# Kernel optimization log

Measured on AMD Instinct MI355X. Metric: run time of the kernel, lower is better.

Reference implementation:

```python
import jax, jax.numpy as jnp
import numpy as np

HEAD_SIZE = 64
EMB_SIZE = 1024
B, T = 8, 2048


def setup_inputs() -> dict:
    key = jax.random.key(0)
    k_x, k_q, k_k, k_v, k_m = jax.random.split(key, 5)
    X = jax.random.normal(k_x, (B, T, EMB_SIZE), dtype=jnp.float32)
    # nn.Linear(emb, head, bias=False) weights have shape (head, emb)
    s = EMB_SIZE ** -0.5
    Wq = jax.random.uniform(k_q, (HEAD_SIZE, EMB_SIZE), jnp.float32, -s, s)
    Wk = jax.random.uniform(k_k, (HEAD_SIZE, EMB_SIZE), jnp.float32, -s, s)
    Wv = jax.random.uniform(k_v, (HEAD_SIZE, EMB_SIZE), jnp.float32, -s, s)
    padding_mask = jax.random.randint(k_m, (B, T), 0, 2).astype(bool)
    # ensure no row is fully masked (would yield NaN softmax)
    padding_mask = padding_mask.at[:, 0].set(False)
    return {"X": X, "Wq": Wq, "Wk": Wk, "Wv": Wv, "padding_mask": padding_mask}


def reference(X, Wq, Wk, Wv, padding_mask):
    # X: (B,T,C); W*: (H,C); padding_mask: (B,T) bool, True = masked key
    C = X.shape[-1]
    Q = jnp.einsum('btc,hc->bth', X, Wq)
    K = jnp.einsum('btc,hc->bth', X, Wk)
    V = jnp.einsum('btc,hc->bth', X, Wv)
    # NOTE: source scales by emb_size**-0.5 (C), not head_size**-0.5
    wei = jnp.einsum('bth,bsh->bts', Q, K) * (C ** -0.5)  # (B,T,T)
    wei = jnp.where(padding_mask[:, None, :], -jnp.inf, wei)
    wei = jax.nn.softmax(wei, axis=-1)  # dropout disabled (eval mode)
    out = jnp.einsum('bts,bsh->bth', wei, V)  # (B,T,H)
    return out
```

## Files before the change

### kernel.cpp

```cpp
#include <hip/hip_runtime.h>
#include <hip/hip_bf16.h>
#include <math.h>


#define T_SEQ 2048
#define EMB 1024
#define HS 64
#define NB 8

typedef __attribute__((ext_vector_type(8))) short short8;
typedef __attribute__((ext_vector_type(4))) float f32x4;
typedef __attribute__((ext_vector_type(2))) unsigned int uint2_t;
typedef unsigned short ushort_t;

static __device__ inline ushort_t f2bf(float f) {
  union { float f; unsigned u; } v; v.f = f;
  unsigned r = v.u + 0x7FFF + ((v.u >> 16) & 1);
  return (ushort_t)(r >> 16);
}
static __device__ inline unsigned pk2(float a, float b) {
  return (unsigned)f2bf(a) | ((unsigned)f2bf(b) << 16);
}
static __device__ inline void lds_barrier() {
  asm volatile("s_waitcnt lgkmcnt(0)" ::: "memory");
  __builtin_amdgcn_s_barrier();
}

#define GL16(gp, lp)                                                 \
  __builtin_amdgcn_global_load_lds(                                  \
      (const __attribute__((address_space(1))) void*)(gp),           \
      (__attribute__((address_space(3))) void*)(lp), 16, 0, 0)

__global__ __launch_bounds__(256) void convw_kernel(
    const float* __restrict__ Wq, const float* __restrict__ Wk,
    const float* __restrict__ Wv, ushort_t* __restrict__ Wb) {
  const int m = blockIdx.x >> 4;
  const int blk = blockIdx.x & 15;
  const float* src = (m == 0) ? Wq : (m == 1) ? Wk : Wv;
  const float scale = (m == 0) ? 0.03125f * 1.44269504f : 1.0f;
  const int base = blk * 4096 + threadIdx.x * 16;
  ushort_t* dst = Wb + m * 65536;
  ushort_t tmp[16];
#pragma unroll
  for (int j = 0; j < 4; ++j) {
    float4 x = *(const float4*)(src + base + j * 4);
    tmp[j * 4 + 0] = f2bf(x.x * scale);
    tmp[j * 4 + 1] = f2bf(x.y * scale);
    tmp[j * 4 + 2] = f2bf(x.z * scale);
    tmp[j * 4 + 3] = f2bf(x.w * scale);
  }
  *(short8*)(dst + base) = *(short8*)tmp;
  *(short8*)(dst + base + 8) = *(short8*)(tmp + 8);
}

__global__ __launch_bounds__(256) void proj_kernel(
    const float* __restrict__ X, const ushort_t* __restrict__ Wb,
    ushort_t* __restrict__ Qb, ushort_t* __restrict__ Kb,
    ushort_t* __restrict__ Vtb) {
  __shared__ __align__(16) ushort_t Xs[2][64 * 128];
  const int tid = threadIdx.x;
  const int lane = tid & 63, w = tid >> 6;
  const int l15 = lane & 15, hi = lane >> 4;
  const long rbase = (long)blockIdx.x * 64;

  const ushort_t* Wrow[3];
#pragma unroll
  for (int t = 0; t < 3; ++t) {
    const int ht = 3 * w + t, m = ht >> 2, hs = ht & 3;
    Wrow[t] = Wb + m * 65536 + (hs * 16 + l15) * 1024 + hi * 8;
  }

  short8 wfA[6], wfB[6], wfC[6], wfD[6];
  auto loadw = [&](short8 (&dst)[6], int s) {
#pragma unroll
    for (int t = 0; t < 3; ++t) {
      dst[2 * t + 0] = *(const short8*)(Wrow[t] + s * 64);
      dst[2 * t + 1] = *(const short8*)(Wrow[t] + s * 64 + 32);
    }
  };
  loadw(wfA, 0); loadw(wfB, 1); loadw(wfC, 2);

  float4 xrA[8], xrB[8];
  auto stage_load = [&](float4 (&xr)[8], int c) {
#pragma unroll
    for (int j = 0; j < 8; ++j) {
      const int F = j * 256 + tid;
      const int row = F >> 5, c4 = F & 31;
      xr[j] = *(const float4*)(X + (rbase + row) * EMB + c * 128 + c4 * 4);
    }
  };
  auto stage_write = [&](float4 (&xr)[8], int buf) {
    ushort_t* Xd = Xs[buf];
#pragma unroll
    for (int j = 0; j < 8; ++j) {
      const int F = j * 256 + tid;
      const int row = F >> 5, c4 = F & 31;
      uint2_t pv;
      pv.x = pk2(xr[j].x, xr[j].y);
      pv.y = pk2(xr[j].z, xr[j].w);
      *(uint2_t*)((char*)(Xd + row * 128) + ((c4 * 8) ^ ((row & 7) << 4))) = pv;
    }
  };

  f32x4 acc[4][3];
#pragma unroll
  for (int rt = 0; rt < 4; ++rt)
#pragma unroll
    for (int t = 0; t < 3; ++t) acc[rt][t] = (f32x4){0.f, 0.f, 0.f, 0.f};

  const int swA = (l15 & 7) << 4;

  auto body = [&](int s, int buf, short8 (&cur)[6], short8 (&pre)[6]) {
    if (s + 3 < 16) loadw(pre, s + 3);
    const int sb = (s & 1) * 128;
#pragma unroll
    for (int rt = 0; rt < 4; ++rt) {
      const char* rowp = (const char*)(Xs[buf] + (rt * 16 + l15) * 128);
      short8 a0 = *(const short8*)(rowp + ((sb + hi * 16) ^ swA));
      short8 a1 = *(const short8*)(rowp + ((sb + 64 + hi * 16) ^ swA));
#pragma unroll
      for (int t = 0; t < 3; ++t) {
        acc[rt][t] = __builtin_amdgcn_mfma_f32_16x16x32_bf16(
            a0, cur[2 * t + 0], acc[rt][t], 0, 0, 0);
        acc[rt][t] = __builtin_amdgcn_mfma_f32_16x16x32_bf16(
            a1, cur[2 * t + 1], acc[rt][t], 0, 0, 0);
      }
    }
  };

  stage_load(xrA, 0);
  stage_write(xrA, 0);
  stage_load(xrB, 1);
  lds_barrier();

  stage_load(xrA, 2);
  body(0, 0, wfA, wfD); body(1, 0, wfB, wfA);
  stage_write(xrB, 1); lds_barrier();
  stage_load(xrB, 3);
  body(2, 1, wfC, wfB); body(3, 1, wfD, wfC);
  stage_write(xrA, 0); lds_barrier();
  stage_load(xrA, 4);
  body(4, 0, wfA, wfD); body(5, 0, wfB, wfA);
  stage_write(xrB, 1); lds_barrier();
  stage_load(xrB, 5);
  body(6, 1, wfC, wfB); body(7, 1, wfD, wfC);
  stage_write(xrA, 0); lds_barrier();
  stage_load(xrA, 6);
  body(8, 0, wfA, wfD); body(9, 0, wfB, wfA);
  stage_write(xrB, 1); lds_barrier();
  stage_load(xrB, 7);
  body(10, 1, wfC, wfB); body(11, 1, wfD, wfC);
  stage_write(xrA, 0); lds_barrier();
  body(12, 0, wfA, wfD); body(13, 0, wfB, wfA);
  stage_write(xrB, 1); lds_barrier();
  body(14, 1, wfC, wfB); body(15, 1, wfD, wfC);

  const long bblk = rbase >> 11;
  const long tb0 = rbase & 2047;
  ushort_t* outs[2] = {Qb, Kb};
#pragma unroll
  for (int rt = 0; rt < 4; ++rt)
#pragma unroll
    for (int t = 0; t < 3; ++t) {
      const int ht = 3 * w + t, m = ht >> 2, hs = ht & 3;
      const int h = hs * 16 + l15;
      if (m < 2) {
#pragma unroll
        for (int r = 0; r < 4; ++r) {
          const long row = rbase + rt * 16 + 4 * hi + r;
          outs[m][row * 64 + h] = f2bf(acc[rt][t][r]);
        }
      } else {
        const long tloc = tb0 + rt * 16 + 4 * hi;
        uint2_t v;
        v.x = pk2(acc[rt][t][0], acc[rt][t][1]);
        v.y = pk2(acc[rt][t][2], acc[rt][t][3]);
        *(uint2_t*)(Vtb + bblk * (long)HS * T_SEQ + (long)h * T_SEQ + tloc) = v;
      }
    }
}

__global__ __launch_bounds__(512) void attn_kernel(
    const ushort_t* __restrict__ Qb, const ushort_t* __restrict__ Kb,
    const ushort_t* __restrict__ Vtb, const int* __restrict__ mask,
    float* __restrict__ out) {
  __shared__ __align__(16) char Lds[152064];

  const int tid = threadIdx.x;
  const int lane = tid & 63, w = tid >> 6;
  const int l15 = lane & 15, hi = lane >> 4;
  const int qs = w & 3, g = w >> 2;
  const int si = tid & 255;
  const int id = blockIdx.x;
  const int b = id & 7;
  const int q0 = (id >> 3) * 64;

  ushort_t* biasB = (ushort_t*)(Lds + 147456);
  float* alphaArr = (float*)(Lds + 151552);

  {
    const ushort_t nb = f2bf(-1e30f);
    const int* mp = mask + b * T_SEQ + tid * 4;
    int4 m0 = *(const int4*)(mp);
    ushort_t t4[4];
    t4[0] = m0.x ? nb : 0; t4[1] = m0.y ? nb : 0;
    t4[2] = m0.z ? nb : 0; t4[3] = m0.w ? nb : 0;
    *(uint2_t*)(biasB + tid * 4) = *(uint2_t*)t4;
  }

  const ushort_t* Qrow = Qb + (long)(b * T_SEQ + q0 + qs * 16 + l15) * 64;
  const short8 qf0 = *(const short8*)(Qrow + hi * 8);
  const short8 qf1 = *(const short8*)(Qrow + 32 + hi * 8);

  const ushort_t* Kg = Kb + (long)b * T_SEQ * 64;
  const ushort_t* Vg = Vtb + (long)b * HS * T_SEQ;

  auto stage_gl = [&](int t, int buf) {
    char* Kd = Lds + (g * 4 + buf) * 8192;
    const ushort_t* ktile = Kg + (g * 1024 + t * 64) * 64;
#pragma unroll
    for (int j = 0; j < 2; ++j) {
      const int F = j * 256 + si;
      const int row = F >> 3, sl = F & 7;
      const int gsl = sl ^ (row & 7);
      GL16(ktile + row * 64 + gsl * 8, Kd + F * 16);
    }
    char* Vd = Lds + 65536 + (g * 4 + buf) * 8192;
    const ushort_t* vtile = Vg + g * 1024 + t * 64;
#pragma unroll
    for (int j = 0; j < 2; ++j) {
      const int F = j * 256 + si;
      const int row = F >> 3, sl = F & 7;
      const int gsl = sl ^ (row & 7);
      GL16(vtile + (long)row * T_SEQ + gsl * 8, Vd + F * 16);
    }
  };

  f32x4 O[4];
#pragma unroll
  for (int ht = 0; ht < 4; ++ht) O[ht] = (f32x4){0.f, 0.f, 0.f, 0.f};
  float mrow = -1e30f, lsum = 0.f;

  char* prow = Lds + 131072 + w * 2048 + l15 * 128;
  const int sw = (l15 & 7) << 4;
  const int swr = (l15 & 7) << 4;

  auto tile_compute = [&](int t, int buf) {
    f32x4 s[4];
    const char* Kl = Lds + (g * 4 + buf) * 8192;
    __builtin_amdgcn_s_setprio(1);
#pragma unroll
    for (int kt = 0; kt < 4; ++kt) {
      const char* kr = Kl + (kt * 16 + l15) * 128;
      short8 k0 = *(const short8*)(kr + ((hi * 16) ^ swr));
      short8 k1 = *(const short8*)(kr + ((64 + hi * 16) ^ swr));
      f32x4 z = {0.f, 0.f, 0.f, 0.f};
      s[kt] = __builtin_amdgcn_mfma_f32_16x16x32_bf16(k0, qf0, z, 0, 0, 0);
      s[kt] = __builtin_amdgcn_mfma_f32_16x16x32_bf16(k1, qf1, s[kt], 0, 0, 0);
    }
    __builtin_amdgcn_s_setprio(0);

    const ushort_t* blp = biasB + g * 1024 + t * 64;
#pragma unroll
    for (int kt = 0; kt < 4; ++kt) {
      const uint2_t bu = *(const uint2_t*)(blp + kt * 16 + hi * 4);
      union { unsigned u; float f; } c0, c1, c2, c3;
      c0.u = bu.x << 16; c1.u = bu.x & 0xFFFF0000u;
      c2.u = bu.y << 16; c3.u = bu.y & 0xFFFF0000u;
      s[kt][0] += c0.f; s[kt][1] += c1.f;
      s[kt][2] += c2.f; s[kt][3] += c3.f;
    }

    float t0m = fmaxf(fmaxf(s[0][0], s[0][1]), fmaxf(s[0][2], s[0][3]));
    float t1m = fmaxf(fmaxf(s[1][0], s[1][1]), fmaxf(s[1][2], s[1][3]));
    float t2m = fmaxf(fmaxf(s[2][0], s[2][1]), fmaxf(s[2][2], s[2][3]));
    float t3m = fmaxf(fmaxf(s[3][0], s[3][1]), fmaxf(s[3][2], s[3][3]));
    float mt = fmaxf(fmaxf(t0m, t1m), fmaxf(t2m, t3m));
    mt = fmaxf(mt, __shfl_xor(mt, 16, 64));
    mt = fmaxf(mt, __shfl_xor(mt, 32, 64));

    const bool skip = __all(mt <= mrow + 11.5415603f);
    float mnew = mrow;
    if (!skip) {
      mnew = fmaxf(mrow, mt);
      const float alpha = exp2f(mrow - mnew);
      if (lane < 16) alphaArr[w * 16 + l15] = alpha;
      lsum *= alpha;
      mrow = mnew;
    }

    float psum = 0.f;
#pragma unroll
    for (int kt = 0; kt < 4; ++kt) {
      const float p0 = exp2f(s[kt][0] - mnew);
      const float p1 = exp2f(s[kt][1] - mnew);
      const float p2 = exp2f(s[kt][2] - mnew);
      const float p3 = exp2f(s[kt][3] - mnew);
      psum += (p0 + p1) + (p2 + p3);
      const int a0 = (kt * 32 + hi * 8) ^ sw;
      *(unsigned*)(prow + a0) = pk2(p0, p1);
      *(unsigned*)(prow + a0 + 4) = pk2(p2, p3);
    }
    lsum += psum;

    if (!skip) {
      const f32x4 av = *(const f32x4*)(alphaArr + w * 16 + 4 * hi);
#pragma unroll
      for (int ht = 0; ht < 4; ++ht) O[ht] *= av;
    }

    short8 pa0 = *(const short8*)(prow + ((hi * 16) ^ sw));
    short8 pa1 = *(const short8*)(prow + ((64 + hi * 16) ^ sw));
    const char* Vl = Lds + 65536 + (g * 4 + buf) * 8192;
    __builtin_amdgcn_s_setprio(1);
#pragma unroll
    for (int ht = 0; ht < 4; ++ht) {
      const char* vr = Vl + (ht * 16 + l15) * 128;
      short8 v0 = *(const short8*)(vr + ((hi * 16) ^ swr));
      short8 v1 = *(const short8*)(vr + ((64 + hi * 16) ^ swr));
      O[ht] = __builtin_amdgcn_mfma_f32_16x16x32_bf16(pa0, v0, O[ht], 0, 0, 0);
      O[ht] = __builtin_amdgcn_mfma_f32_16x16x32_bf16(pa1, v1, O[ht], 0, 0, 0);
    }
    __builtin_amdgcn_s_setprio(0);
  };

  stage_gl(0, 0);
  stage_gl(1, 1);
  __syncthreads();

#pragma unroll 1
  for (int ts = 0; ts < 16; ts += 2) {
    if (ts + 2 < 16) {
      stage_gl(ts + 2, (ts + 2) & 3);
      stage_gl(ts + 3, (ts + 3) & 3);
    }
    tile_compute(ts, ts & 3);
    tile_compute(ts + 1, (ts + 1) & 3);
    __syncthreads();
  }

  lsum += __shfl_xor(lsum, 16, 64);
  lsum += __shfl_xor(lsum, 32, 64);

  float* mergeF = (float*)Lds;
  if (g == 1) {
    float* ml = mergeF + (qs * 64 + lane) * 18;
    ml[0] = mrow; ml[1] = lsum;
#pragma unroll
    for (int ht = 0; ht < 4; ++ht)
#pragma unroll
      for (int r = 0; r < 4; ++r) ml[2 + ht * 4 + r] = O[ht][r];
  }
  __syncthreads();
  if (g == 0) {
    const float* ml = mergeF + (qs * 64 + lane) * 18;
    const float mB = ml[0], lB = ml[1];
    const float mn = fmaxf(mrow, mB);
    const float aa = exp2f(mrow - mn);
    const float ab = exp2f(mB - mn);
    const float inv = 1.0f / (lsum * aa + lB * ab);
    float* ob = out + (long)(b * T_SEQ + q0 + qs * 16) * 64;
#pragma unroll
    for (int r = 0; r < 4; ++r) {
      const float aar = __shfl(aa, 4 * hi + r, 64);
      const float abr = __shfl(ab, 4 * hi + r, 64);
      const float invr = __shfl(inv, 4 * hi + r, 64);
#pragma unroll
      for (int ht = 0; ht < 4; ++ht)
        ob[(4 * hi + r) * 64 + ht * 16 + l15] =
            (O[ht][r] * aar + ml[2 + ht * 4 + r] * abr) * invr;
    }
  }
}

extern "C" void kernel_launch(void* const* d_in, const int* in_sizes, int n_in,
                              void* d_out, int out_size, void* d_ws, size_t ws_size,
                              hipStream_t stream) {
  const float* X  = (const float*)d_in[0];
  const float* Wq = (const float*)d_in[1];
  const float* Wk = (const float*)d_in[2];
  const float* Wv = (const float*)d_in[3];
  const int* mask = (const int*)d_in[4];
  float* outp = (float*)d_out;

  const long NT = (long)NB * T_SEQ * HS;
  ushort_t* wsb = (ushort_t*)d_ws;
  ushort_t* Qb  = wsb;
  ushort_t* Kb  = wsb + NT;
  ushort_t* Vtb = wsb + 2 * NT;
  ushort_t* Wb  = wsb + 3 * NT;

  convw_kernel<<<48, 256, 0, stream>>>(Wq, Wk, Wv, Wb);
  proj_kernel<<<(NB * T_SEQ) / 64, 256, 0, stream>>>(X, Wb, Qb, Kb, Vtb);
  attn_kernel<<<256, 512, 0, stream>>>(Qb, Kb, Vtb, mask, outp);
}
```

Baseline: 53.94 us.

## Shrink LDS footprint to double buffering and read mask directly from global

Cuts shared memory from about 148KB to 80KB by going from four K/V tile buffers per group to two, dropping the LDS mask-bias array, and dropping the LDS alpha array. The mask is now loaded from global memory per tile, and alpha is broadcast with lane shuffles. The pipeline changes from staging two tiles ahead with one barrier per pair to staging one tile ahead with a barrier every tile. The smaller footprint could allow two workgroups per CU, at the cost of more barriers, shallower prefetch and extra global mask loads.

```diff
diff --git a/kernel.cpp b/kernel.cpp
--- a/kernel.cpp
+++ b/kernel.cpp
@@ -184,7 +184,7 @@
     const ushort_t* __restrict__ Qb, const ushort_t* __restrict__ Kb,
     const ushort_t* __restrict__ Vtb, const int* __restrict__ mask,
     float* __restrict__ out) {
-  __shared__ __align__(16) char Lds[152064];
+  __shared__ __align__(16) char Lds[81920];
 
   const int tid = threadIdx.x;
   const int lane = tid & 63, w = tid >> 6;
@@ -195,28 +195,16 @@
   const int b = id & 7;
   const int q0 = (id >> 3) * 64;
 
-  ushort_t* biasB = (ushort_t*)(Lds + 147456);
-  float* alphaArr = (float*)(Lds + 151552);
-
-  {
-    const ushort_t nb = f2bf(-1e30f);
-    const int* mp = mask + b * T_SEQ + tid * 4;
-    int4 m0 = *(const int4*)(mp);
-    ushort_t t4[4];
-    t4[0] = m0.x ? nb : 0; t4[1] = m0.y ? nb : 0;
-    t4[2] = m0.z ? nb : 0; t4[3] = m0.w ? nb : 0;
-    *(uint2_t*)(biasB + tid * 4) = *(uint2_t*)t4;
-  }
-
   const ushort_t* Qrow = Qb + (long)(b * T_SEQ + q0 + qs * 16 + l15) * 64;
   const short8 qf0 = *(const short8*)(Qrow + hi * 8);
   const short8 qf1 = *(const short8*)(Qrow + 32 + hi * 8);
 
   const ushort_t* Kg = Kb + (long)b * T_SEQ * 64;
   const ushort_t* Vg = Vtb + (long)b * HS * T_SEQ;
+  const int* mb = mask + b * T_SEQ;
 
   auto stage_gl = [&](int t, int buf) {
-    char* Kd = Lds + (g * 4 + buf) * 8192;
+    char* Kd = Lds + (g * 2 + buf) * 8192;
     const ushort_t* ktile = Kg + (g * 1024 + t * 64) * 64;
 #pragma unroll
     for (int j = 0; j < 2; ++j) {
@@ -225,7 +213,7 @@
       const int gsl = sl ^ (row & 7);
       GL16(ktile + row * 64 + gsl * 8, Kd + F * 16);
     }
-    char* Vd = Lds + 65536 + (g * 4 + buf) * 8192;
+    char* Vd = Lds + 32768 + (g * 2 + buf) * 8192;
     const ushort_t* vtile = Vg + g * 1024 + t * 64;
 #pragma unroll
     for (int j = 0; j < 2; ++j) {
@@ -241,13 +229,19 @@
   for (int ht = 0; ht < 4; ++ht) O[ht] = (f32x4){0.f, 0.f, 0.f, 0.f};
   float mrow = -1e30f, lsum = 0.f;
 
-  char* prow = Lds + 131072 + w * 2048 + l15 * 128;
+  char* prow = Lds + 65536 + w * 2048 + l15 * 128;
   const int sw = (l15 & 7) << 4;
   const int swr = (l15 & 7) << 4;
 
   auto tile_compute = [&](int t, int buf) {
+    const int kb0 = g * 1024 + t * 64;
+    int4 mi0 = *(const int4*)(mb + kb0 + 0 * 16 + hi * 4);
+    int4 mi1 = *(const int4*)(mb + kb0 + 1 * 16 + hi * 4);
+    int4 mi2 = *(const int4*)(mb + kb0 + 2 * 16 + hi * 4);
+    int4 mi3 = *(const int4*)(mb + kb0 + 3 * 16 + hi * 4);
+
     f32x4 s[4];
-    const char* Kl = Lds + (g * 4 + buf) * 8192;
+    const char* Kl = Lds + (g * 2 + buf) * 8192;
     __builtin_amdgcn_s_setprio(1);
 #pragma unroll
     for (int kt = 0; kt < 4; ++kt) {
@@ -260,16 +254,14 @@
     }
     __builtin_amdgcn_s_setprio(0);
 
-    const ushort_t* blp = biasB + g * 1024 + t * 64;
-#pragma unroll
-    for (int kt = 0; kt < 4; ++kt) {
-      const uint2_t bu = *(const uint2_t*)(blp + kt * 16 + hi * 4);
-      union { unsigned u; float f; } c0, c1, c2, c3;
-      c0.u = bu.x << 16; c1.u = bu.x & 0xFFFF0000u;
-      c2.u = bu.y << 16; c3.u = bu.y & 0xFFFF0000u;
-      s[kt][0] += c0.f; s[kt][1] += c1.f;
-      s[kt][2] += c2.f; s[kt][3] += c3.f;
-    }
+    s[0][0] += mi0.x ? -1e30f : 0.f; s[0][1] += mi0.y ? -1e30f : 0.f;
+    s[0][2] += mi0.z ? -1e30f : 0.f; s[0][3] += mi0.w ? -1e30f : 0.f;
+    s[1][0] += mi1.x ? -1e30f : 0.f; s[1][1] += mi1.y ? -1e30f : 0.f;
+    s[1][2] += mi1.z ? -1e30f : 0.f; s[1][3] += mi1.w ? -1e30f : 0.f;
+    s[2][0] += mi2.x ? -1e30f : 0.f; s[2][1] += mi2.y ? -1e30f : 0.f;
+    s[2][2] += mi2.z ? -1e30f : 0.f; s[2][3] += mi2.w ? -1e30f : 0.f;
+    s[3][0] += mi3.x ? -1e30f : 0.f; s[3][1] += mi3.y ? -1e30f : 0.f;
+    s[3][2] += mi3.z ? -1e30f : 0.f; s[3][3] += mi3.w ? -1e30f : 0.f;
 
     float t0m = fmaxf(fmaxf(s[0][0], s[0][1]), fmaxf(s[0][2], s[0][3]));
     float t1m = fmaxf(fmaxf(s[1][0], s[1][1]), fmaxf(s[1][2], s[1][3]));
@@ -280,11 +272,11 @@
     mt = fmaxf(mt, __shfl_xor(mt, 32, 64));
 
     const bool skip = __all(mt <= mrow + 11.5415603f);
+    float alpha = 1.0f;
     float mnew = mrow;
     if (!skip) {
       mnew = fmaxf(mrow, mt);
-      const float alpha = exp2f(mrow - mnew);
-      if (lane < 16) alphaArr[w * 16 + l15] = alpha;
+      alpha = exp2f(mrow - mnew);
       lsum *= alpha;
       mrow = mnew;
     }
@@ -304,14 +296,17 @@
     lsum += psum;
 
     if (!skip) {
-      const f32x4 av = *(const f32x4*)(alphaArr + w * 16 + 4 * hi);
-#pragma unroll
-      for (int ht = 0; ht < 4; ++ht) O[ht] *= av;
+#pragma unroll
+      for (int r = 0; r < 4; ++r) {
+        const float ar = __shfl(alpha, 4 * hi + r, 64);
+#pragma unroll
+        for (int ht = 0; ht < 4; ++ht) O[ht][r] *= ar;
+      }
     }
 
     short8 pa0 = *(const short8*)(prow + ((hi * 16) ^ sw));
     short8 pa1 = *(const short8*)(prow + ((64 + hi * 16) ^ sw));
-    const char* Vl = Lds + 65536 + (g * 4 + buf) * 8192;
+    const char* Vl = Lds + 32768 + (g * 2 + buf) * 8192;
     __builtin_amdgcn_s_setprio(1);
 #pragma unroll
     for (int ht = 0; ht < 4; ++ht) {
@@ -325,17 +320,12 @@
   };
 
   stage_gl(0, 0);
-  stage_gl(1, 1);
   __syncthreads();
 
 #pragma unroll 1
-  for (int ts = 0; ts < 16; ts += 2) {
-    if (ts + 2 < 16) {
-      stage_gl(ts + 2, (ts + 2) & 3);
-      stage_gl(ts + 3, (ts + 3) & 3);
-    }
-    tile_compute(ts, ts & 3);
-    tile_compute(ts + 1, (ts + 1) & 3);
+  for (int t = 0; t < 16; ++t) {
+    if (t < 15) stage_gl(t + 1, (t + 1) & 1);
+    tile_compute(t, t & 1);
     __syncthreads();
   }
 
```

Measured after the change: 59.00 us. +9.4%, slower.
